# Kernel tuning notes

Measured on AMD Instinct MI355X. Metric: run time of the kernel, lower is better.

## Reference

```python
import jax, jax.numpy as jnp
import numpy as np

H = 12  # max_heads

def setup_inputs() -> dict:
    key = jax.random.key(0)
    ks = jax.random.split(key, 5)
    B, N, E = 8, 1024, 768
    return {
        "x": jax.random.normal(ks[0], (B, N, E), dtype=jnp.float32),
        "w_qkv": jax.random.normal(ks[1], (3 * E, E), dtype=jnp.float32) * 0.02,
        "b_qkv": jax.random.normal(ks[2], (3 * E,), dtype=jnp.float32) * 0.02,
        "w_proj": jax.random.normal(ks[3], (E, E), dtype=jnp.float32) * 0.02,
        "b_proj": jax.random.normal(ks[4], (E,), dtype=jnp.float32) * 0.02,
        "active_heads": 8,
    }

def reference(x, w_qkv, b_qkv, w_proj, b_proj, active_heads):
    B, N, E = x.shape
    D = E // H
    scale = D ** -0.5
    # qkv projection: [B,N,3E] -> [3,B,H,N,D]
    qkv = (x @ w_qkv.T + b_qkv).reshape(B, N, 3, H, D)
    qkv = jnp.transpose(qkv, (2, 0, 3, 1, 4))
    q, k, v = qkv[0], qkv[1], qkv[2]
    # head mask from active_heads (static int)
    head_mask = (jnp.arange(H) < active_heads).astype(x.dtype)
    m = head_mask[None, :, None, None]
    q = q * m
    k = k * m
    v = v * m
    attn = jax.nn.softmax(jnp.einsum("bhqd,bhkd->bhqk", q, k) * scale, axis=-1)
    out = jnp.einsum("bhqk,bhkd->bhqd", attn, v)
    out = jnp.transpose(out, (0, 2, 1, 3)).reshape(B, N, E)
    channel_mask = jnp.repeat(head_mask, D)  # [E]
    out = out * channel_mask[None, None, :]
    return out @ w_proj.T + b_proj
```

## Files before the change

kernel.cpp:

```cpp
#include <hip/hip_runtime.h>
#include <hip/hip_fp16.h>

#define NH 12
#define BSZ 8
#define NSEQ 1024
#define EDIM 768
#define DH 64

typedef _Float16 f16;
typedef f16 half8 __attribute__((ext_vector_type(8)));
typedef f16 half4 __attribute__((ext_vector_type(4)));
typedef float f32x4 __attribute__((ext_vector_type(4)));
typedef unsigned int u32;
typedef u32 u32x2 __attribute__((ext_vector_type(2)));

static __device__ __forceinline__ void gload16(const void* g, void* l) {
    __builtin_amdgcn_global_load_lds((const __attribute__((address_space(1))) u32*)g,
                                     (__attribute__((address_space(3))) u32*)l, 16, 0, 0);
}
static __device__ __forceinline__ u32 pkrtz(float a, float b) {
    auto h = __builtin_amdgcn_cvt_pkrtz(a, b);
    return __builtin_bit_cast(u32, h);
}
#define MFMA16(a, b, c) __builtin_amdgcn_mfma_f32_16x16x32_f16((a), (b), (c), 0, 0, 0)

__global__ void cvt_all_kernel(const float* __restrict__ x, const float* __restrict__ wq,
                               const float* __restrict__ wp, f16* __restrict__ dst) {
    const int NX = BSZ * NSEQ * EDIM;
    const int NWQ = 3 * EDIM * EDIM;
    int i = (blockIdx.x * blockDim.x + threadIdx.x) * 4;
    const float* s;
    int j;
    if (i < NX) { s = x; j = i; }
    else if (i < NX + NWQ) { s = wq; j = i - NX; }
    else { s = wp; j = i - NX - NWQ; }
    float4 v = *(const float4*)(s + j);
    half4 o = { (f16)v.x, (f16)v.y, (f16)v.z, (f16)v.w };
    *(half4*)(dst + i) = o;
}

template<int MODE>
__global__ __launch_bounds__(256) void gemm_kernel(
    const f16* __restrict__ A, const f16* __restrict__ Wt, const float* __restrict__ bias,
    f16* __restrict__ qbuf, f16* __restrict__ kbuf, f16* __restrict__ vbuf,
    float* __restrict__ outp, const int* __restrict__ activep, int K, int NC)
{
    __shared__ __align__(16) f16 Lds[4][4][4][64][8];

    const int tid = threadIdx.x;
    const int c0 = blockIdx.x * 128;
    const int m0 = blockIdx.y * 128;
    if (MODE == 0) {
        int hb = (c0 % EDIM) >> 6;
        if (hb >= *activep) return;
    }
    const int lane = tid & 63;
    const int wid  = tid >> 6;
    const int wr = wid >> 1, wc = wid & 1;
    const int r16 = lane & 15, rg = lane >> 4;

    f32x4 acc[4][4];
#pragma unroll
    for (int i = 0; i < 4; ++i)
#pragma unroll
        for (int j = 0; j < 4; ++j)
            acc[i][j] = f32x4{0.f, 0.f, 0.f, 0.f};

    const f16* srcbase = (wid < 2) ? (A  + (size_t)(m0 + (wid & 1) * 64) * K)
                                   : (Wt + (size_t)(c0 + (wid & 1) * 64) * K);
    const f16* gsrc = srcbase + (size_t)r16 * K + rg * 8;
    const int nkt = K / 32;

    auto stage = [&](int buf, int kt) {
#pragma unroll
        for (int f = 0; f < 4; ++f)
            gload16(gsrc + (size_t)(f * 16) * K + kt * 32, &Lds[buf][wid][f][0][0]);
    };

    stage(0, 0);
    if (nkt > 1) stage(1, 1);
#pragma unroll 1
    for (int kt = 0; kt < nkt; ++kt) {
        if (kt + 2 < nkt) {
            stage((kt + 2) & 3, kt + 2);
            asm volatile("s_waitcnt vmcnt(8)" ::: "memory");
        } else if (kt + 1 < nkt) {
            asm volatile("s_waitcnt vmcnt(4)" ::: "memory");
        } else {
            asm volatile("s_waitcnt vmcnt(0)" ::: "memory");
        }
        __builtin_amdgcn_s_barrier();
        __builtin_amdgcn_sched_barrier(0);
        const int cur = kt & 3;
        half8 af[4], bf[4];
#pragma unroll
        for (int f = 0; f < 4; ++f) {
            af[f] = *(const half8*)&Lds[cur][wr][f][lane][0];
            bf[f] = *(const half8*)&Lds[cur][2 + wc][f][lane][0];
        }
        __builtin_amdgcn_s_setprio(1);
#pragma unroll
        for (int fm = 0; fm < 4; ++fm)
#pragma unroll
            for (int fn = 0; fn < 4; ++fn)
                acc[fm][fn] = MFMA16(af[fm], bf[fn], acc[fm][fn]);
        __builtin_amdgcn_s_setprio(0);
    }

#pragma unroll
    for (int fn = 0; fn < 4; ++fn) {
        const int c = c0 + wc * 64 + fn * 16 + r16;
        const float bv = bias[c];
#pragma unroll
        for (int fm = 0; fm < 4; ++fm) {
            const int mbase = m0 + wr * 64 + fm * 16 + rg * 4;
#pragma unroll
            for (int r = 0; r < 4; ++r) {
                const float val = acc[fm][fn][r] + bv;
                const int m = mbase + r;
                if (MODE == 1) {
                    outp[(size_t)m * EDIM + c] = val;
                } else {
                    const int s  = c / EDIM;
                    const int cc = c % EDIM;
                    const int hh = cc >> 6, d = cc & 63;
                    const int bb = m >> 10, n = m & 1023;
                    f16* dst = (s == 0) ? qbuf : ((s == 1) ? kbuf : vbuf);
                    dst[(((size_t)bb * NH + hh) * NSEQ + n) * DH + d] = (f16)val;
                }
            }
        }
    }
}

__global__ __launch_bounds__(256) void vtrans_kernel(const f16* __restrict__ vbuf,
                                                     f16* __restrict__ vtb,
                                                     const int* __restrict__ activep) {
    const int b = blockIdx.z, h = blockIdx.y;
    if (h >= *activep) return;
    const int n0 = blockIdx.x * 64;
    __shared__ __align__(16) f16 T[64][72];
    const f16* src = vbuf + (((size_t)b * NH + h) * NSEQ + n0) * DH;
    f16* dst = vtb + ((size_t)b * NH + h) * DH * NSEQ;
    const int t = threadIdx.x;
    const int rn = t >> 2, rc = t & 3;
    *(half8*)&T[rn][rc * 16]     = *(const half8*)&src[(size_t)rn * DH + rc * 16];
    *(half8*)&T[rn][rc * 16 + 8] = *(const half8*)&src[(size_t)rn * DH + rc * 16 + 8];
    __syncthreads();
    const int d = t >> 2, nc = (t & 3) * 16;
    half8 o0, o1;
#pragma unroll
    for (int j = 0; j < 8; ++j) {
        o0[j] = T[nc + j][d];
        o1[j] = T[nc + 8 + j][d];
    }
    *(half8*)&dst[(size_t)d * NSEQ + n0 + nc]     = o0;
    *(half8*)&dst[(size_t)d * NSEQ + n0 + nc + 8] = o1;
}

__global__ __launch_bounds__(256) void attn_kernel(
    const f16* __restrict__ qbuf, const f16* __restrict__ kbuf, const f16* __restrict__ vtb,
    f16* __restrict__ ctx, const int* __restrict__ activep)
{
    __shared__ __align__(16) f16 Kh[2][64][64];
    __shared__ __align__(16) f16 Vh[2][64][64];
    __shared__ __align__(16) f16 Ph[4][16][64];

    const int b = blockIdx.z, h = blockIdx.y;
    const int q0 = blockIdx.x * 64;
    const int tid = threadIdx.x, lane = tid & 63, wid = tid >> 6;

    if (h >= *activep) {
        const int r = tid >> 2, cp = tid & 3;
        half8 z = { (f16)0,(f16)0,(f16)0,(f16)0,(f16)0,(f16)0,(f16)0,(f16)0 };
        size_t base = ((size_t)b * NSEQ + q0 + r) * EDIM + h * DH + cp * 16;
        *(half8*)&ctx[base]     = z;
        *(half8*)&ctx[base + 8] = z;
        return;
    }

    const size_t hb = (((size_t)b * NH + h) * NSEQ) * DH;
    const f16* Q  = qbuf + hb;
    const char* Kp = (const char*)(kbuf + hb);
    const char* Vp = (const char*)(vtb + hb);

    const int ql = lane & 15;
    const int g  = lane >> 4;
    const int q7 = ql & 7;

    half8 qb0, qb1;
    {
        const f16* qp = Q + (size_t)(q0 + wid * 16 + ql) * DH + g * 8;
        qb0 = *(const half8*)qp        * (f16)0.125f;
        qb1 = *(const half8*)(qp + 32) * (f16)0.125f;
    }

    const int srow8 = lane >> 3;
    const int schk  = (lane & 7) ^ srow8;

    auto stage = [&](int buf, int kt) {
        const char* kb = Kp + (size_t)kt * 8192;
#pragma unroll
        for (int i = 0; i < 2; ++i) {
            const int r = wid * 16 + i * 8 + srow8;
            gload16(kb + (size_t)r * 128 + schk * 16, &Kh[buf][wid * 16 + i * 8][0]);
            gload16(Vp + (size_t)r * (NSEQ * 2) + (size_t)kt * 128 + schk * 16,
                    &Vh[buf][wid * 16 + i * 8][0]);
        }
    };

    f32x4 oacc[4];
#pragma unroll
    for (int i = 0; i < 4; ++i) oacc[i] = f32x4{0.f, 0.f, 0.f, 0.f};
    float mr = -INFINITY, lr = 0.f;

    char* prow = (char*)&Ph[wid][ql][0];

    stage(0, 0);
    const int NT = NSEQ / 64;
    for (int kt = 0; kt < NT; ++kt) {
        const int cur = kt & 1;
        __syncthreads();
        if (kt + 1 < NT) stage(cur ^ 1, kt + 1);

        f32x4 st[4];
        __builtin_amdgcn_s_setprio(1);
#pragma unroll
        for (int s = 0; s < 4; ++s) {
            f32x4 t = f32x4{0.f, 0.f, 0.f, 0.f};
            t = MFMA16(*(const half8*)((const char*)&Kh[cur][16 * s + ql][0] + ((g ^ q7) << 4)),       qb0, t);
            t = MFMA16(*(const half8*)((const char*)&Kh[cur][16 * s + ql][0] + (((4 | g) ^ q7) << 4)), qb1, t);
            st[s] = t;
        }
        __builtin_amdgcn_s_setprio(0);

        float pmax;
        {
            float m0v = fmaxf(fmaxf(st[0][0], st[0][1]), fmaxf(st[0][2], st[0][3]));
            float m1v = fmaxf(fmaxf(st[1][0], st[1][1]), fmaxf(st[1][2], st[1][3]));
            float m2v = fmaxf(fmaxf(st[2][0], st[2][1]), fmaxf(st[2][2], st[2][3]));
            float m3v = fmaxf(fmaxf(st[3][0], st[3][1]), fmaxf(st[3][2], st[3][3]));
            pmax = fmaxf(fmaxf(m0v, m1v), fmaxf(m2v, m3v));
        }
        pmax = fmaxf(pmax, __shfl_xor(pmax, 16));
        pmax = fmaxf(pmax, __shfl_xor(pmax, 32));
        const float mnew = fmaxf(mr, pmax);
        const float sc = __expf(mr - mnew);
        float psum = 0.f;
#pragma unroll
        for (int s = 0; s < 4; ++s)
#pragma unroll
            for (int r = 0; r < 4; ++r) {
                float p = __expf(st[s][r] - mnew);
                st[s][r] = p;
                psum += p;
            }
        psum += __shfl_xor(psum, 16);
        psum += __shfl_xor(psum, 32);
        lr = lr * sc + psum;
        mr = mnew;

#pragma unroll
        for (int r = 0; r < 4; ++r) {
            const float scr = __shfl(sc, (g << 2) | r);
            oacc[0][r] *= scr; oacc[1][r] *= scr; oacc[2][r] *= scr; oacc[3][r] *= scr;
        }

#pragma unroll
        for (int s = 0; s < 4; ++s) {
            u32x2 w = { pkrtz(st[s][0], st[s][1]), pkrtz(st[s][2], st[s][3]) };
            *(u32x2*)(prow + ((32 * s + 8 * g) ^ (q7 << 4))) = w;
        }
        const half8 pa0 = *(const half8*)(prow + ((16 * g) ^ (q7 << 4)));
        const half8 pa1 = *(const half8*)(prow + ((64 + 16 * g) ^ (q7 << 4)));

        __builtin_amdgcn_s_setprio(1);
#pragma unroll
        for (int db = 0; db < 4; ++db) {
            oacc[db] = MFMA16(pa0, *(const half8*)((const char*)&Vh[cur][16 * db + ql][0] + ((g ^ q7) << 4)),       oacc[db]);
            oacc[db] = MFMA16(pa1, *(const half8*)((const char*)&Vh[cur][16 * db + ql][0] + (((4 | g) ^ q7) << 4)), oacc[db]);
        }
        __builtin_amdgcn_s_setprio(0);
    }

#pragma unroll
    for (int r = 0; r < 4; ++r) {
        const float li = 1.0f / __shfl(lr, (g << 2) | r);
        const int n = q0 + wid * 16 + (g << 2) + r;
#pragma unroll
        for (int db = 0; db < 4; ++db)
            ctx[((size_t)b * NSEQ + n) * EDIM + h * DH + db * 16 + ql] = (f16)(oacc[db][r] * li);
    }
}

extern "C" void kernel_launch(void* const* d_in, const int* in_sizes, int n_in,
                              void* d_out, int out_size, void* d_ws, size_t ws_size,
                              hipStream_t stream) {
    const float* x      = (const float*)d_in[0];
    const float* w_qkv  = (const float*)d_in[1];
    const float* b_qkv  = (const float*)d_in[2];
    const float* w_proj = (const float*)d_in[3];
    const float* b_proj = (const float*)d_in[4];
    const int*   active = (const int*)d_in[5];
    float* out = (float*)d_out;

    char* ws = (char*)d_ws;
    const size_t n_x  = (size_t)BSZ * NSEQ * EDIM;
    const size_t n_wq = (size_t)3 * EDIM * EDIM;
    const size_t n_wp = (size_t)EDIM * EDIM;
    const size_t n_hd = (size_t)BSZ * NH * NSEQ * DH;

    f16* xh   = (f16*)ws;
    f16* wqh  = xh + n_x;
    f16* wph  = wqh + n_wq;
    f16* qh   = wph + n_wp;
    f16* kh   = qh + n_hd;
    f16* vh   = kh + n_hd;
    f16* ctxh = vh + n_hd;
    f16* vtb  = xh;

    const size_t n_cvt = n_x + n_wq + n_wp;
    cvt_all_kernel<<<(int)(n_cvt / 4 / 256), 256, 0, stream>>>(x, w_qkv, w_proj, xh);

    gemm_kernel<0><<<dim3(3 * EDIM / 128, BSZ * NSEQ / 128), 256, 0, stream>>>(
        xh, wqh, b_qkv, qh, kh, vh, nullptr, active, EDIM, 3 * EDIM);

    vtrans_kernel<<<dim3(NSEQ / 64, NH, BSZ), 256, 0, stream>>>(vh, vtb, active);

    attn_kernel<<<dim3(NSEQ / 64, NH, BSZ), 256, 0, stream>>>(qh, kh, vtb, ctxh, active);

    gemm_kernel<1><<<dim3(EDIM / 128, BSZ * NSEQ / 128), 256, 0, stream>>>(
        ctxh, wph, b_proj, nullptr, nullptr, nullptr, out, active, EDIM, EDIM);
}
```

Measured before the change: 135.6 us.

## Enlarge GEMM tiles to 128x256 with 8 waves, XCD-aware block mapping

```diff
diff --git a/kernel.cpp b/kernel.cpp
--- a/kernel.cpp
+++ b/kernel.cpp
@@ -40,23 +40,33 @@
 }
 
 template<int MODE>
-__global__ __launch_bounds__(256) void gemm_kernel(
+__global__ __launch_bounds__(512) void gemm_kernel(
     const f16* __restrict__ A, const f16* __restrict__ Wt, const float* __restrict__ bias,
     f16* __restrict__ qbuf, f16* __restrict__ kbuf, f16* __restrict__ vbuf,
-    float* __restrict__ outp, const int* __restrict__ activep, int K, int NC)
+    float* __restrict__ outp, const int* __restrict__ activep, int Kd, int NCd)
 {
-    __shared__ __align__(16) f16 Lds[4][4][4][64][8];
-
+    __shared__ __align__(16) f16 Ah[2][2][4][64][8];
+    __shared__ __align__(16) f16 Bh[2][4][4][64][8];
+
+    constexpr int K = EDIM;
+    constexpr int NKT = K / 32;
+    constexpr int NB = (MODE == 0) ? 9 : 3;
+
+    const int lin = blockIdx.x;
+    const int xcd = lin & 7, pos = lin >> 3;
+    const int bx = pos % NB;
+    const int my = xcd + (pos / NB) * 8;
+    const int c0 = bx * 256;
+    const int m0 = my * 128;
+    const int ah = *activep;
+    if (MODE == 0) {
+        if (((c0 % EDIM) >> 6) >= ah) return;
+    }
     const int tid = threadIdx.x;
-    const int c0 = blockIdx.x * 128;
-    const int m0 = blockIdx.y * 128;
-    if (MODE == 0) {
-        int hb = (c0 % EDIM) >> 6;
-        if (hb >= *activep) return;
-    }
     const int lane = tid & 63;
     const int wid  = tid >> 6;
-    const int wr = wid >> 1, wc = wid & 1;
+    const int wr = wid >> 2;
+    const int wc = wid & 3;
     const int r16 = lane & 15, rg = lane >> 4;
 
     f32x4 acc[4][4];
@@ -66,38 +76,39 @@
         for (int j = 0; j < 4; ++j)
             acc[i][j] = f32x4{0.f, 0.f, 0.f, 0.f};
 
-    const f16* srcbase = (wid < 2) ? (A  + (size_t)(m0 + (wid & 1) * 64) * K)
-                                   : (Wt + (size_t)(c0 + (wid & 1) * 64) * K);
-    const f16* gsrc = srcbase + (size_t)r16 * K + rg * 8;
-    const int nkt = K / 32;
+    const int awrh = wid >> 2, afm = wid & 3;
+    const int ib0 = 2 * wid, ib1 = 2 * wid + 1;
+    const f16* gAs  = A  + (size_t)(m0 + awrh * 64 + afm * 16 + r16) * K + rg * 8;
+    const f16* gBs0 = Wt + (size_t)(c0 + (ib0 >> 2) * 64 + (ib0 & 3) * 16 + r16) * K + rg * 8;
+    const f16* gBs1 = Wt + (size_t)(c0 + (ib1 >> 2) * 64 + (ib1 & 3) * 16 + r16) * K + rg * 8;
 
     auto stage = [&](int buf, int kt) {
-#pragma unroll
-        for (int f = 0; f < 4; ++f)
-            gload16(gsrc + (size_t)(f * 16) * K + kt * 32, &Lds[buf][wid][f][0][0]);
+        gload16(gAs  + kt * 32, &Ah[buf][awrh][afm][0][0]);
+        gload16(gBs0 + kt * 32, &Bh[buf][ib0 >> 2][ib0 & 3][0][0]);
+        gload16(gBs1 + kt * 32, &Bh[buf][ib1 >> 2][ib1 & 3][0][0]);
     };
 
     stage(0, 0);
-    if (nkt > 1) stage(1, 1);
+    stage(1, 1);
+    asm volatile("s_waitcnt vmcnt(3)" ::: "memory");
+    __builtin_amdgcn_s_barrier();
+    __builtin_amdgcn_sched_barrier(0);
+
 #pragma unroll 1
-    for (int kt = 0; kt < nkt; ++kt) {
-        if (kt + 2 < nkt) {
-            stage((kt + 2) & 3, kt + 2);
-            asm volatile("s_waitcnt vmcnt(8)" ::: "memory");
-        } else if (kt + 1 < nkt) {
-            asm volatile("s_waitcnt vmcnt(4)" ::: "memory");
-        } else {
-            asm volatile("s_waitcnt vmcnt(0)" ::: "memory");
-        }
+    for (int kt = 0; kt < NKT; ++kt) {
+        const int cur = kt & 1;
+        half8 af[4], bf[4];
+#pragma unroll
+        for (int f = 0; f < 4; ++f) {
+            af[f] = *(const half8*)&Ah[cur][wr][f][lane][0];
+            bf[f] = *(const half8*)&Bh[cur][wc][f][lane][0];
+        }
+        asm volatile("s_waitcnt lgkmcnt(0)" ::: "memory");
+        __builtin_amdgcn_sched_barrier(0);
         __builtin_amdgcn_s_barrier();
         __builtin_amdgcn_sched_barrier(0);
-        const int cur = kt & 3;
-        half8 af[4], bf[4];
-#pragma unroll
-        for (int f = 0; f < 4; ++f) {
-            af[f] = *(const half8*)&Lds[cur][wr][f][lane][0];
-            bf[f] = *(const half8*)&Lds[cur][2 + wc][f][lane][0];
-        }
+        if (kt + 2 < NKT) stage(cur, kt + 2);
+        __builtin_amdgcn_sched_barrier(0);
         __builtin_amdgcn_s_setprio(1);
 #pragma unroll
         for (int fm = 0; fm < 4; ++fm)
@@ -105,12 +116,19 @@
             for (int fn = 0; fn < 4; ++fn)
                 acc[fm][fn] = MFMA16(af[fm], bf[fn], acc[fm][fn]);
         __builtin_amdgcn_s_setprio(0);
+        if (kt + 1 < NKT) {
+            if (kt + 2 < NKT) asm volatile("s_waitcnt vmcnt(3)" ::: "memory");
+            else              asm volatile("s_waitcnt vmcnt(0)" ::: "memory");
+            __builtin_amdgcn_s_barrier();
+            __builtin_amdgcn_sched_barrier(0);
+        }
     }
 
 #pragma unroll
     for (int fn = 0; fn < 4; ++fn) {
         const int c = c0 + wc * 64 + fn * 16 + r16;
         const float bv = bias[c];
+        const bool colActive = (MODE == 1) || (((c % EDIM) >> 6) < ah);
 #pragma unroll
         for (int fm = 0; fm < 4; ++fm) {
             const int mbase = m0 + wr * 64 + fm * 16 + rg * 4;
@@ -120,7 +138,7 @@
                 const int m = mbase + r;
                 if (MODE == 1) {
                     outp[(size_t)m * EDIM + c] = val;
-                } else {
+                } else if (colActive) {
                     const int s  = c / EDIM;
                     const int cc = c % EDIM;
                     const int hh = cc >> 6, d = cc & 63;
@@ -322,13 +340,13 @@
     const size_t n_cvt = n_x + n_wq + n_wp;
     cvt_all_kernel<<<(int)(n_cvt / 4 / 256), 256, 0, stream>>>(x, w_qkv, w_proj, xh);
 
-    gemm_kernel<0><<<dim3(3 * EDIM / 128, BSZ * NSEQ / 128), 256, 0, stream>>>(
+    gemm_kernel<0><<<dim3(64 * 9), 512, 0, stream>>>(
         xh, wqh, b_qkv, qh, kh, vh, nullptr, active, EDIM, 3 * EDIM);
 
     vtrans_kernel<<<dim3(NSEQ / 64, NH, BSZ), 256, 0, stream>>>(vh, vtb, active);
 
     attn_kernel<<<dim3(NSEQ / 64, NH, BSZ), 256, 0, stream>>>(qh, kh, vtb, ctxh, active);
 
-    gemm_kernel<1><<<dim3(EDIM / 128, BSZ * NSEQ / 128), 256, 0, stream>>>(
+    gemm_kernel<1><<<dim3(64 * 3), 512, 0, stream>>>(
         ctxh, wph, b_proj, nullptr, nullptr, nullptr, out, active, EDIM, EDIM);
 }
```

New measurement: 129.4 us. -4.6%, faster.
